# Kernel tuning notes

Measured on AMD Instinct MI355X. Metric: run time of the kernel, lower is better.

Reference implementation:

```python
import jax, jax.numpy as jnp
import numpy as np

B_SZ = 512; S = 3; F = 5; C = 62; E = 5
D_MODEL = C * E * F          # 1550
N_LAYERS = 2
D_STATE = 16
EXPAND = 2
D_CONV = 4
ED = EXPAND * D_MODEL        # 3100
DT_RANK = (D_MODEL + 15) // 16  # 97
VOCAB = 128
EPS = 1e-5


def setup_inputs() -> dict:
    key = jax.random.key(0)
    ks = jax.random.split(key, 10)
    def g(i, shape, scale=0.02):
        return jax.random.normal(ks[i], shape, dtype=jnp.float32) * scale
    A_log = jnp.tile(jnp.log(jnp.arange(1, D_STATE + 1, dtype=jnp.float32))[None, None, :],
                     (N_LAYERS, ED, 1))
    return {
        "x": jax.random.normal(ks[0], (B_SZ, S, F, C, E), dtype=jnp.float32),
        "in_proj_w": g(1, (N_LAYERS, 2 * ED, D_MODEL)),
        "conv_w": g(2, (N_LAYERS, ED, 1, D_CONV), 0.1),
        "conv_b": jnp.zeros((N_LAYERS, ED), jnp.float32),
        "x_proj_w": g(3, (N_LAYERS, DT_RANK + 2 * D_STATE, ED)),
        "dt_proj_w": g(4, (N_LAYERS, ED, DT_RANK), 0.1),
        "dt_proj_b": jnp.full((N_LAYERS, ED), -4.6, jnp.float32),  # softplus ~ 0.01
        "A_log": A_log,
        "D_param": jnp.ones((N_LAYERS, ED), jnp.float32),
        "out_proj_w": g(5, (N_LAYERS, D_MODEL, ED)),
        "norm_w": jnp.ones((N_LAYERS, D_MODEL), jnp.float32),
        "normf_w": jnp.ones((D_MODEL,), jnp.float32),
        "lm_head_w": g(6, (VOCAB, D_MODEL)),
        "bn_w": jnp.ones((F,), jnp.float32),
        "bn_b": jnp.zeros((F,), jnp.float32),
        "emb_w": g(7, (256, VOCAB)),
        "emb_b": jnp.zeros((256,), jnp.float32),
    }


def _rmsnorm(x, w):
    return x * jax.lax.rsqrt(jnp.mean(x * x, axis=-1, keepdims=True) + EPS) * w


def _silu(x):
    return x * jax.nn.sigmoid(x)


def _causal_conv(xt, w, b):
    # xt: (B, ED, L); w: (ED, 1, K) depthwise causal conv (pad K-1 left)
    y = jax.lax.conv_general_dilated(xt, w, (1,), [(D_CONV - 1, 0)],
                                     feature_group_count=ED)
    return y + b[None, :, None]


def _ssm_scan(deltaA, deltaBx, Cm):
    # deltaA, deltaBx: (B, L, ED, N); Cm: (B, L, N)
    def step(h, inp):
        dA, dBx, c = inp
        h = dA * h + dBx                      # (B, ED, N)
        y = jnp.einsum('ben,bn->be', h, c)    # (B, ED)
        return h, y
    h0 = jnp.zeros((deltaA.shape[0], ED, D_STATE), deltaA.dtype)
    xs = (deltaA.transpose(1, 0, 2, 3), deltaBx.transpose(1, 0, 2, 3), Cm.transpose(1, 0, 2))
    _, ys = jax.lax.scan(step, h0, xs)
    return ys.transpose(1, 0, 2)              # (B, L, ED)


def _mixer(h, in_w, cw, cb, xp_w, dt_w, dt_b, A_log, Dp, out_w):
    # h: (B, L, D_MODEL)
    xz = jnp.einsum('bld,ed->ble', h, in_w)   # (B, L, 2*ED)
    x_in, z = jnp.split(xz, 2, axis=-1)
    xc = _silu(_causal_conv(x_in.transpose(0, 2, 1), cw, cb).transpose(0, 2, 1))  # (B,L,ED)
    dbc = jnp.einsum('ble,re->blr', xc, xp_w)  # (B, L, DT_RANK + 2N)
    dt = dbc[..., :DT_RANK]
    Bm = dbc[..., DT_RANK:DT_RANK + D_STATE]
    Cm = dbc[..., DT_RANK + D_STATE:]
    delta = jax.nn.softplus(jnp.einsum('blr,er->ble', dt, dt_w) + dt_b)  # (B,L,ED)
    A = -jnp.exp(A_log)                       # (ED, N)
    deltaA = jnp.exp(delta[..., None] * A)                       # (B,L,ED,N)
    deltaBx = delta[..., None] * Bm[:, :, None, :] * xc[..., None]
    y = _ssm_scan(deltaA, deltaBx, Cm) + Dp * xc
    return jnp.einsum('ble,de->bld', y * _silu(z), out_w)


def reference(x, in_proj_w, conv_w, conv_b, x_proj_w, dt_proj_w, dt_proj_b,
              A_log, D_param, out_proj_w, norm_w, normf_w, lm_head_w,
              bn_w, bn_b, emb_w, emb_b):
    b, s, f, c, e = x.shape
    fx = x.transpose(0, 1, 3, 2, 4).reshape(b, s, c * f * e)  # (B, S, D_MODEL)
    h = fx
    for l in range(N_LAYERS):
        h = h + _mixer(_rmsnorm(h, norm_w[l]), in_proj_w[l], conv_w[l], conv_b[l],
                       x_proj_w[l], dt_proj_w[l], dt_proj_b[l], A_log[l],
                       D_param[l], out_proj_w[l])
    h = _rmsnorm(h, normf_w)
    logits = jnp.einsum('bsd,vd->bsv', h, lm_head_w)          # (B, S, 128)
    m = jnp.broadcast_to(logits[:, None], (b, f, s, VOCAB))    # repeat over f
    # BatchNorm2d(feature_dim) in training mode: stats over (B, S, VOCAB) per channel f
    mean = jnp.mean(m, axis=(0, 2, 3), keepdims=True)
    var = jnp.var(m, axis=(0, 2, 3), keepdims=True)
    mn = (m - mean) * jax.lax.rsqrt(var + EPS)
    mn = mn * bn_w[None, :, None, None] + bn_b[None, :, None, None]
    return jnp.einsum('bfsv,ov->bfso', mn, emb_w) + emb_b      # (B, F, S, 256)
```

## Files before the change

kernel.cpp:

```cpp
#include <hip/hip_runtime.h>
#include <hip/hip_bf16.h>
#include <math.h>

#define B_SZ 512
#define SEQ 3
#define D_MODEL 1550
#define ED 3100
#define NSTATE 16
#define DTR 97
#define DBC_R 129
#define VOCAB 128
#define NBS (B_SZ*SEQ)
#define EPSV 1e-5f

#define KD 1600
#define KE 3136
#define NIP 6272
#define NXP 256
#define NOP 1664
#define NDT 3200
#define KDT 128
#define DBC_LD 256

#define QIP 2508800
#define QXP 200704
#define QDT 102400
#define QOP 1304576
#define AEL 49600
#define QDB 98304
#define QLM 51200
#define QLG 49152
#define TEL 32768
#define PREP_N0 4397762
#define PREP_N1 4264384

static inline int cdiv_h(int a, int b){ return (a + b - 1) / b; }

__device__ __forceinline__ float silu_f(float x){ return x / (1.0f + expf(-x)); }

using bf16x8 = __attribute__((ext_vector_type(8))) short;
using f32x4  = __attribute__((ext_vector_type(4))) float;

__device__ __forceinline__ void gload16(const void* g, void* l){
  __builtin_amdgcn_global_load_lds(
      (const __attribute__((address_space(1))) unsigned int*)g,
      (__attribute__((address_space(3))) unsigned int*)l,
      16, 0, 0);
}

__global__ void k_permute(const float* __restrict__ x, float* __restrict__ h){
  int idx = blockIdx.x * 256 + threadIdx.x;
  if (idx >= NBS * D_MODEL) return;
  int d = idx % D_MODEL;
  int row = idx / D_MODEL;
  int e = d % 5;
  int f = (d / 5) % 5;
  int c = d / 25;
  h[idx] = x[(((size_t)row * 5 + f) * 62 + c) * 5 + e];
}

__device__ __forceinline__ void cast4(const float* __restrict__ src,
                                      __hip_bfloat16* __restrict__ dst,
                                      int q, int N, int K, int Kp){
  int i4 = q * 4;
  int row = i4 / Kp;
  int col = i4 % Kp;
  const float* srow = src + (size_t)row * K;
  #pragma unroll
  for (int j = 0; j < 4; j++){
    int c = col + j;
    float v = (row < N && c < K) ? srow[c] : 0.f;
    dst[i4 + j] = __float2bfloat16(v);
  }
}

__global__ __launch_bounds__(256)
void k_prep(const float* __restrict__ ipw, const float* __restrict__ xpw,
            const float* __restrict__ dtw, const float* __restrict__ opw,
            const float* __restrict__ alog,
            const float* __restrict__ lmw, const float* __restrict__ embw,
            __hip_bfloat16* __restrict__ ipb, __hip_bfloat16* __restrict__ xpb,
            __hip_bfloat16* __restrict__ dtwb, __hip_bfloat16* __restrict__ opb,
            float* __restrict__ A_t, float* __restrict__ dbc,
            __hip_bfloat16* __restrict__ lmb, float* __restrict__ logits,
            float* __restrict__ emb_t, float* __restrict__ sumw,
            float* __restrict__ stats, int l0){
  int idx = blockIdx.x * 256 + threadIdx.x;
  if (idx < QIP){ cast4(ipw, ipb, idx, 2 * ED, D_MODEL, KD); return; } idx -= QIP;
  if (idx < QXP){ cast4(xpw, xpb, idx, DBC_R, ED, KE); return; } idx -= QXP;
  if (idx < QDT){ cast4(dtw, dtwb, idx, ED, DTR, KDT); return; } idx -= QDT;
  if (idx < QOP){ cast4(opw, opb, idx, D_MODEL, ED, KE); return; } idx -= QOP;
  if (idx < AEL){
    int n = idx / ED, ch = idx % ED;
    A_t[idx] = -expf(alog[(size_t)ch * NSTATE + n]);
    return;
  } idx -= AEL;
  if (idx < QDB){
    int i4 = idx * 4;
    dbc[i4] = 0.f; dbc[i4+1] = 0.f; dbc[i4+2] = 0.f; dbc[i4+3] = 0.f;
    return;
  } idx -= QDB;
  if (!l0) return;
  if (idx < QLM){ cast4(lmw, lmb, idx, VOCAB, D_MODEL, KD); return; } idx -= QLM;
  if (idx < QLG){
    int i4 = idx * 4;
    logits[i4] = 0.f; logits[i4+1] = 0.f; logits[i4+2] = 0.f; logits[i4+3] = 0.f;
    return;
  } idx -= QLG;
  if (idx < TEL){
    int v = idx >> 8, o = idx & 255;
    emb_t[idx] = embw[(size_t)o * VOCAB + v];
    return;
  } idx -= TEL;
  if (idx < 256){
    const float* r = embw + (size_t)idx * VOCAB;
    float s = 0.f;
    for (int v = 0; v < VOCAB; v++) s += r[v];
    sumw[idx] = s;
    return;
  } idx -= 256;
  if (idx < 2) stats[idx] = 0.f;
}

__global__ void k_rmsnorm_bf16(const float* __restrict__ in, const float* __restrict__ w,
                               __hip_bfloat16* __restrict__ out, int D, int Kp){
  int row = blockIdx.x;
  const float* xr = in + (size_t)row * D;
  float ss = 0.f;
  for (int i = threadIdx.x; i < D; i += blockDim.x){ float v = xr[i]; ss = fmaf(v, v, ss); }
  __shared__ float red[4];
  __shared__ float sscale;
  int lane = threadIdx.x & 63, wv = threadIdx.x >> 6;
  #pragma unroll
  for (int o = 32; o > 0; o >>= 1) ss += __shfl_down(ss, o, 64);
  if (lane == 0) red[wv] = ss;
  __syncthreads();
  if (threadIdx.x == 0){
    float t = red[0] + red[1] + red[2] + red[3];
    sscale = 1.0f / sqrtf(t / (float)D + EPSV);
  }
  __syncthreads();
  float sc = sscale;
  __hip_bfloat16* orow = out + (size_t)row * Kp;
  for (int i = threadIdx.x; i < Kp; i += blockDim.x){
    float v = (i < D) ? xr[i] * sc * w[i] : 0.f;
    orow[i] = __float2bfloat16(v);
  }
}

__global__ void k_cast_dbc(const float* __restrict__ dbc, __hip_bfloat16* __restrict__ dst){
  int idx = blockIdx.x * 256 + threadIdx.x;
  if (idx >= NBS * KDT) return;
  int row = idx >> 7;
  int c = idx & 127;
  float v = (c < DTR) ? dbc[(size_t)row * DBC_LD + c] : 0.f;
  dst[idx] = __float2bfloat16(v);
}

template<int SPLITS, bool ATOMIC, bool OUT_BF16>
__global__ __launch_bounds__(256)
void k_gemm2(const __hip_bfloat16* __restrict__ A, const __hip_bfloat16* __restrict__ B,
             void* Cv, int Kp, int Nld, int Nreal){
  __shared__ short Al[2][4096];
  __shared__ short Bl[2][4096];
  const int gx = gridDim.x, gy = gridDim.y;
  const int nwg = gx * gy;
  const int wg = blockIdx.y * gx + blockIdx.x;
  const int q = nwg >> 3, r = nwg & 7;
  const int xcd = wg & 7, off = wg >> 3;
  const int nid = (xcd < r ? xcd * (q + 1) : r * (q + 1) + (xcd - r) * q) + off;
  const int bm = (nid % gy) * 128;
  const int bn = (nid / gy) * 128;

  const int t = threadIdx.x;
  const int tt8 = t * 8;

  int kb = 0, ke = Kp;
  if (SPLITS > 1){
    int Kc = ((Kp / SPLITS + 31) / 32) * 32;
    kb = blockIdx.z * Kc;
    ke = min(kb + Kc, Kp);
    if (kb >= ke) return;
  }
  const int nt = (ke - kb) / 32;

  const short* Ab = (const short*)A;
  const short* Bb = (const short*)B;
  const short* ga0 = Ab + (size_t)(bm + (t >> 2)) * Kp + (t & 3) * 8;
  const short* ga1 = Ab + (size_t)(bm + 64 + (t >> 2)) * Kp + (t & 3) * 8;
  const short* gb0 = Bb + (size_t)(bn + (t >> 2)) * Kp + (t & 3) * 8;
  const short* gb1 = Bb + (size_t)(bn + 64 + (t >> 2)) * Kp + (t & 3) * 8;

  const int l = t & 63;
  const int wid = t >> 6;
  const int wr = wid >> 1, wc = wid & 1;
  const int fr = l & 15;
  const int ko = (l >> 4) * 8;

  f32x4 acc[4][4] = {};

#define STAGE(buf, kof) do{ \
    gload16(ga0 + (kof), &Al[buf][tt8]); \
    gload16(ga1 + (kof), &Al[buf][2048 + tt8]); \
    gload16(gb0 + (kof), &Bl[buf][tt8]); \
    gload16(gb1 + (kof), &Bl[buf][2048 + tt8]); }while(0)

  STAGE(0, kb);
  __syncthreads();
  int cur = 0;
  for (int it = 0; it < nt; ++it){
    if (it + 1 < nt) STAGE(cur ^ 1, kb + (it + 1) * 32);
    bf16x8 af[4], bfr[4];
    #pragma unroll
    for (int m = 0; m < 4; m++)
      af[m] = *(const bf16x8*)&Al[cur][(wr * 64 + m * 16 + fr) * 32 + ko];
    #pragma unroll
    for (int n = 0; n < 4; n++)
      bfr[n] = *(const bf16x8*)&Bl[cur][(wc * 64 + n * 16 + fr) * 32 + ko];
    #pragma unroll
    for (int m = 0; m < 4; m++)
      #pragma unroll
      for (int n = 0; n < 4; n++)
        acc[m][n] = __builtin_amdgcn_mfma_f32_16x16x32_bf16(af[m], bfr[n], acc[m][n], 0, 0, 0);
    if (it + 1 < nt){ __syncthreads(); cur ^= 1; }
  }
#undef STAGE

  float* Cf = (float*)Cv;
  __hip_bfloat16* Cb = (__hip_bfloat16*)Cv;
  const int r0 = (l >> 4) * 4;
  #pragma unroll
  for (int m = 0; m < 4; m++){
    #pragma unroll
    for (int n = 0; n < 4; n++){
      int col = bn + wc * 64 + n * 16 + fr;
      if (col < Nreal){
        size_t base = (size_t)(bm + wr * 64 + m * 16 + r0) * Nld + col;
        #pragma unroll
        for (int j = 0; j < 4; j++){
          float v = acc[m][n][j];
          size_t o = base + (size_t)j * Nld;
          if (OUT_BF16)      Cb[o] = __float2bfloat16(v);
          else if (ATOMIC)   atomicAdd(&Cf[o], v);
          else               Cf[o] = v;
        }
      }
    }
  }
}

__global__ void k_conv_silu(const __hip_bfloat16* __restrict__ xz, const float* __restrict__ cw,
                            const float* __restrict__ cb, float* __restrict__ xc_f,
                            __hip_bfloat16* __restrict__ xc_b){
  int idx = blockIdx.x * 256 + threadIdx.x;
  if (idx >= B_SZ * KE) return;
  int ch = idx % KE;
  int b  = idx / KE;
  size_t ob = (size_t)b * SEQ * KE + ch;
  if (ch >= ED){
    __hip_bfloat16 z = __float2bfloat16(0.f);
    xc_b[ob] = z; xc_b[ob + KE] = z; xc_b[ob + 2 * KE] = z;
    return;
  }
  const __hip_bfloat16* base = xz + (size_t)b * SEQ * NIP + ch;
  float x0 = __bfloat162float(base[0]);
  float x1 = __bfloat162float(base[NIP]);
  float x2 = __bfloat162float(base[2 * NIP]);
  const float* w = cw + (size_t)ch * 4;
  float w1 = w[1], w2 = w[2], w3 = w[3];
  float bb = cb[ch];
  float s0 = silu_f(fmaf(w3, x0, bb));
  float s1 = silu_f(fmaf(w2, x0, fmaf(w3, x1, bb)));
  float s2 = silu_f(fmaf(w1, x0, fmaf(w2, x1, fmaf(w3, x2, bb))));
  size_t of = (size_t)b * SEQ * ED + ch;
  xc_f[of]          = s0;
  xc_f[of + ED]     = s1;
  xc_f[of + 2 * ED] = s2;
  xc_b[ob]          = __float2bfloat16(s0);
  xc_b[ob + KE]     = __float2bfloat16(s1);
  xc_b[ob + 2 * KE] = __float2bfloat16(s2);
}

__global__ __launch_bounds__(256)
void k_scan2(const __hip_bfloat16* __restrict__ delta_b, const float* __restrict__ dbc,
             const float* __restrict__ dtb, const float* __restrict__ A_t,
             const float* __restrict__ Dp, const __hip_bfloat16* __restrict__ xz,
             const float* __restrict__ xc_f, __hip_bfloat16* __restrict__ xc_b){
  __shared__ float sB[SEQ][NSTATE], sC[SEQ][NSTATE];
  int b = blockIdx.y;
  if (threadIdx.x < SEQ * 2 * NSTATE){
    int t = threadIdx.x / (2 * NSTATE), r = threadIdx.x % (2 * NSTATE);
    float v = dbc[(size_t)(b * SEQ + t) * DBC_LD + DTR + r];
    if (r < NSTATE) sB[t][r] = v; else sC[t][r - NSTATE] = v;
  }
  __syncthreads();
  int ch = blockIdx.x * 256 + threadIdx.x;
  if (ch >= ED) return;

  float bias = dtb[ch];
  float dlt[SEQ];
  #pragma unroll
  for (int t = 0; t < SEQ; t++){
    float acc = __bfloat162float(delta_b[(size_t)(b * SEQ + t) * NDT + ch]) + bias;
    dlt[t] = (acc > 20.f) ? acc : log1pf(expf(acc));
  }

  size_t of = (size_t)b * SEQ * ED + ch;
  float xcv[SEQ] = { xc_f[of], xc_f[of + ED], xc_f[of + 2 * ED] };
  float y[SEQ] = {0.f, 0.f, 0.f};
  #pragma unroll
  for (int n = 0; n < NSTATE; n++){
    float Av = A_t[(size_t)n * ED + ch];
    float hs = 0.f;
    #pragma unroll
    for (int t = 0; t < SEQ; t++){
      float dA = expf(dlt[t] * Av);
      hs = fmaf(dA, hs, dlt[t] * sB[t][n] * xcv[t]);
      y[t] = fmaf(hs, sC[t][n], y[t]);
    }
  }
  float dp = Dp[ch];
  const __hip_bfloat16* zbase = xz + (size_t)b * SEQ * NIP + ED + ch;
  size_t ob = (size_t)b * SEQ * KE + ch;
  #pragma unroll
  for (int t = 0; t < SEQ; t++){
    float z = __bfloat162float(zbase[(size_t)t * NIP]);
    float yy = fmaf(dp, xcv[t], y[t]);
    xc_b[ob + (size_t)t * KE] = __float2bfloat16(yy * silu_f(z));
  }
}

__global__ __launch_bounds__(256)
void k_stats_part(const float* __restrict__ logits, float* __restrict__ stats){
  float s = 0.f, ss = 0.f;
  for (int i = blockIdx.x * 256 + threadIdx.x; i < NBS * VOCAB; i += gridDim.x * 256){
    float v = logits[i]; s += v; ss = fmaf(v, v, ss);
  }
  #pragma unroll
  for (int o = 32; o > 0; o >>= 1){ s += __shfl_down(s, o, 64); ss += __shfl_down(ss, o, 64); }
  __shared__ float rs[4], rss[4];
  int lane = threadIdx.x & 63, wv = threadIdx.x >> 6;
  if (lane == 0){ rs[wv] = s; rss[wv] = ss; }
  __syncthreads();
  if (threadIdx.x == 0){
    atomicAdd(&stats[0], rs[0] + rs[1] + rs[2] + rs[3]);
    atomicAdd(&stats[1], rss[0] + rss[1] + rss[2] + rss[3]);
  }
}

__global__ __launch_bounds__(256)
void k_projfinal(const float* __restrict__ logits, const float* __restrict__ emb_t,
                 const float* __restrict__ sumw, const float* __restrict__ stats,
                 const float* __restrict__ bnw, const float* __restrict__ bnb,
                 const float* __restrict__ embb, float* __restrict__ out){
  __shared__ float row[VOCAB];
  int r = blockIdx.x;
  int o = threadIdx.x;
  if (o < VOCAB) row[o] = logits[(size_t)r * VOCAB + o];
  __syncthreads();
  float p = 0.f;
  #pragma unroll 8
  for (int v = 0; v < VOCAB; v++) p = fmaf(row[v], emb_t[v * 256 + o], p);
  const float invN = 1.0f / (float)(NBS * VOCAB);
  float mean = stats[0] * invN;
  float var  = stats[1] * invN - mean * mean;
  float rstd = rsqrtf(var + EPSV);
  int b = r / SEQ, s = r % SEQ;
  float sw = sumw[o];
  float base = rstd * (p - mean * sw);
  float eb = embb[o];
  #pragma unroll
  for (int f = 0; f < 5; f++){
    out[(((size_t)(b * 5 + f)) * SEQ + s) * 256 + o] = bnw[f] * base + bnb[f] * sw + eb;
  }
}

extern "C" void kernel_launch(void* const* d_in, const int* in_sizes, int n_in,
                              void* d_out, int out_size, void* d_ws, size_t ws_size,
                              hipStream_t stream) {
  const float* x          = (const float*)d_in[0];
  const float* in_proj_w  = (const float*)d_in[1];
  const float* conv_w     = (const float*)d_in[2];
  const float* conv_b     = (const float*)d_in[3];
  const float* x_proj_w   = (const float*)d_in[4];
  const float* dt_proj_w  = (const float*)d_in[5];
  const float* dt_proj_b  = (const float*)d_in[6];
  const float* A_log      = (const float*)d_in[7];
  const float* D_param    = (const float*)d_in[8];
  const float* out_proj_w = (const float*)d_in[9];
  const float* norm_w     = (const float*)d_in[10];
  const float* normf_w    = (const float*)d_in[11];
  const float* lm_head_w  = (const float*)d_in[12];
  const float* bn_w       = (const float*)d_in[13];
  const float* bn_b       = (const float*)d_in[14];
  const float* emb_w      = (const float*)d_in[15];
  const float* emb_b      = (const float*)d_in[16];

  float* ws = (float*)d_ws;
  float* h      = ws;
  float* xc_f   = h      + (size_t)NBS * D_MODEL;
  float* dbc    = xc_f   + (size_t)NBS * ED;
  float* logits = dbc    + (size_t)NBS * DBC_LD;
  float* sumw   = logits + (size_t)NBS * VOCAB;
  float* stats  = sumw   + 256;
  float* A_t    = stats  + 2;
  float* emb_t  = A_t    + (size_t)NSTATE * ED;
  __hip_bfloat16* xz_b   = (__hip_bfloat16*)(emb_t + (size_t)VOCAB * 256);
  __hip_bfloat16* hn_b   = xz_b   + (size_t)NBS * NIP;
  __hip_bfloat16* xc_b   = hn_b   + (size_t)NBS * KD;
  __hip_bfloat16* dbc_b  = xc_b   + (size_t)NBS * KE;
  __hip_bfloat16* dlt_b  = dbc_b  + (size_t)NBS * KDT;
  __hip_bfloat16* ipb    = dlt_b  + (size_t)NBS * NDT;
  __hip_bfloat16* xpb    = ipb    + (size_t)NIP * KD;
  __hip_bfloat16* dtwb   = xpb    + (size_t)NXP * KE;
  __hip_bfloat16* opb    = dtwb   + (size_t)NDT * KDT;
  __hip_bfloat16* lmb    = opb    + (size_t)NOP * KE;
  size_t need = (size_t)((char*)(lmb + (size_t)VOCAB * KD) - (char*)ws);
  if (ws_size < need) return;

  k_permute<<<cdiv_h(NBS * D_MODEL, 256), 256, 0, stream>>>(x, h);

  for (int l = 0; l < 2; l++){
    const float* ipw = in_proj_w  + (size_t)l * 2 * ED * D_MODEL;
    const float* cw  = conv_w     + (size_t)l * ED * 4;
    const float* cb  = conv_b     + (size_t)l * ED;
    const float* xpw = x_proj_w   + (size_t)l * DBC_R * ED;
    const float* dtw = dt_proj_w  + (size_t)l * ED * DTR;
    const float* dtb = dt_proj_b  + (size_t)l * ED;
    const float* al  = A_log      + (size_t)l * ED * NSTATE;
    const float* dp  = D_param    + (size_t)l * ED;
    const float* opw = out_proj_w + (size_t)l * D_MODEL * ED;
    const float* nw  = norm_w     + (size_t)l * D_MODEL;

    k_prep<<<cdiv_h(l == 0 ? PREP_N0 : PREP_N1, 256), 256, 0, stream>>>(
        ipw, xpw, dtw, opw, al, lm_head_w, emb_w,
        ipb, xpb, dtwb, opb, A_t, dbc, lmb, logits, emb_t, sumw, stats, l == 0 ? 1 : 0);

    k_rmsnorm_bf16<<<NBS, 256, 0, stream>>>(h, nw, hn_b, D_MODEL, KD);

    k_gemm2<1, false, true><<<dim3(NIP / 128, NBS / 128, 1), 256, 0, stream>>>(
        hn_b, ipb, xz_b, KD, NIP, NIP);

    k_conv_silu<<<cdiv_h(B_SZ * KE, 256), 256, 0, stream>>>(xz_b, cw, cb, xc_f, xc_b);

    k_gemm2<8, true, false><<<dim3(NXP / 128, NBS / 128, 8), 256, 0, stream>>>(
        xc_b, xpb, dbc, KE, DBC_LD, DBC_LD);

    k_cast_dbc<<<cdiv_h(NBS * KDT, 256), 256, 0, stream>>>(dbc, dbc_b);
    k_gemm2<1, false, true><<<dim3(NDT / 128, NBS / 128, 1), 256, 0, stream>>>(
        dbc_b, dtwb, dlt_b, KDT, NDT, NDT);

    k_scan2<<<dim3(cdiv_h(ED, 256), B_SZ), 256, 0, stream>>>(
        dlt_b, dbc, dtb, A_t, dp, xz_b, xc_f, xc_b);

    k_gemm2<2, true, false><<<dim3(NOP / 128, NBS / 128, 2), 256, 0, stream>>>(
        xc_b, opb, h, KE, D_MODEL, D_MODEL);
  }

  k_rmsnorm_bf16<<<NBS, 256, 0, stream>>>(h, normf_w, hn_b, D_MODEL, KD);
  k_gemm2<4, true, false><<<dim3(1, NBS / 128, 4), 256, 0, stream>>>(
      hn_b, lmb, logits, KD, VOCAB, VOCAB);

  k_stats_part<<<192, 256, 0, stream>>>(logits, stats);
  k_projfinal<<<NBS, 256, 0, stream>>>(logits, emb_t, sumw, stats,
                                       bn_w, bn_b, emb_b, (float*)d_out);
}
```

Measured before the change: 550.7 us.

## Swizzle GEMM LDS layout, replace atomic split-K with partial buffers, drop fp32 xc

After: 570.3 us. 3.6% more time.

```diff
diff --git a/kernel.cpp b/kernel.cpp
--- a/kernel.cpp
+++ b/kernel.cpp
@@ -27,12 +27,10 @@
 #define QDT 102400
 #define QOP 1304576
 #define AEL 49600
-#define QDB 98304
 #define QLM 51200
-#define QLG 49152
 #define TEL 32768
-#define PREP_N0 4397762
-#define PREP_N1 4264384
+#define PREP_N1 4166080
+#define PREP_N0 4250306
 
 static inline int cdiv_h(int a, int b){ return (a + b - 1) / b; }
 
@@ -81,8 +79,8 @@
             const float* __restrict__ lmw, const float* __restrict__ embw,
             __hip_bfloat16* __restrict__ ipb, __hip_bfloat16* __restrict__ xpb,
             __hip_bfloat16* __restrict__ dtwb, __hip_bfloat16* __restrict__ opb,
-            float* __restrict__ A_t, float* __restrict__ dbc,
-            __hip_bfloat16* __restrict__ lmb, float* __restrict__ logits,
+            float* __restrict__ A_t,
+            __hip_bfloat16* __restrict__ lmb,
             float* __restrict__ emb_t, float* __restrict__ sumw,
             float* __restrict__ stats, int l0){
   int idx = blockIdx.x * 256 + threadIdx.x;
@@ -95,18 +93,8 @@
     A_t[idx] = -expf(alog[(size_t)ch * NSTATE + n]);
     return;
   } idx -= AEL;
-  if (idx < QDB){
-    int i4 = idx * 4;
-    dbc[i4] = 0.f; dbc[i4+1] = 0.f; dbc[i4+2] = 0.f; dbc[i4+3] = 0.f;
-    return;
-  } idx -= QDB;
   if (!l0) return;
   if (idx < QLM){ cast4(lmw, lmb, idx, VOCAB, D_MODEL, KD); return; } idx -= QLM;
-  if (idx < QLG){
-    int i4 = idx * 4;
-    logits[i4] = 0.f; logits[i4+1] = 0.f; logits[i4+2] = 0.f; logits[i4+3] = 0.f;
-    return;
-  } idx -= QLG;
   if (idx < TEL){
     int v = idx >> 8, o = idx & 255;
     emb_t[idx] = embw[(size_t)o * VOCAB + v];
@@ -148,16 +136,7 @@
   }
 }
 
-__global__ void k_cast_dbc(const float* __restrict__ dbc, __hip_bfloat16* __restrict__ dst){
-  int idx = blockIdx.x * 256 + threadIdx.x;
-  if (idx >= NBS * KDT) return;
-  int row = idx >> 7;
-  int c = idx & 127;
-  float v = (c < DTR) ? dbc[(size_t)row * DBC_LD + c] : 0.f;
-  dst[idx] = __float2bfloat16(v);
-}
-
-template<int SPLITS, bool ATOMIC, bool OUT_BF16>
+template<int SPLITS, bool ATOMIC, bool OUT_BF16, bool PARTIAL>
 __global__ __launch_bounds__(256)
 void k_gemm2(const __hip_bfloat16* __restrict__ A, const __hip_bfloat16* __restrict__ B,
              void* Cv, int Kp, int Nld, int Nreal){
@@ -184,18 +163,19 @@
   }
   const int nt = (ke - kb) / 32;
 
+  const int cg = ((t & 3) ^ ((t >> 2) & 3)) * 8;
   const short* Ab = (const short*)A;
   const short* Bb = (const short*)B;
-  const short* ga0 = Ab + (size_t)(bm + (t >> 2)) * Kp + (t & 3) * 8;
-  const short* ga1 = Ab + (size_t)(bm + 64 + (t >> 2)) * Kp + (t & 3) * 8;
-  const short* gb0 = Bb + (size_t)(bn + (t >> 2)) * Kp + (t & 3) * 8;
-  const short* gb1 = Bb + (size_t)(bn + 64 + (t >> 2)) * Kp + (t & 3) * 8;
+  const short* ga0 = Ab + (size_t)(bm + (t >> 2)) * Kp + cg;
+  const short* ga1 = Ab + (size_t)(bm + 64 + (t >> 2)) * Kp + cg;
+  const short* gb0 = Bb + (size_t)(bn + (t >> 2)) * Kp + cg;
+  const short* gb1 = Bb + (size_t)(bn + 64 + (t >> 2)) * Kp + cg;
 
   const int l = t & 63;
   const int wid = t >> 6;
   const int wr = wid >> 1, wc = wid & 1;
   const int fr = l & 15;
-  const int ko = (l >> 4) * 8;
+  const int cc = ((l >> 4) ^ (l & 3)) * 8;
 
   f32x4 acc[4][4] = {};
 
@@ -213,10 +193,10 @@
     bf16x8 af[4], bfr[4];
     #pragma unroll
     for (int m = 0; m < 4; m++)
-      af[m] = *(const bf16x8*)&Al[cur][(wr * 64 + m * 16 + fr) * 32 + ko];
+      af[m] = *(const bf16x8*)&Al[cur][(wr * 64 + m * 16 + fr) * 32 + cc];
     #pragma unroll
     for (int n = 0; n < 4; n++)
-      bfr[n] = *(const bf16x8*)&Bl[cur][(wc * 64 + n * 16 + fr) * 32 + ko];
+      bfr[n] = *(const bf16x8*)&Bl[cur][(wc * 64 + n * 16 + fr) * 32 + cc];
     #pragma unroll
     for (int m = 0; m < 4; m++)
       #pragma unroll
@@ -228,6 +208,8 @@
 
   float* Cf = (float*)Cv;
   __hip_bfloat16* Cb = (__hip_bfloat16*)Cv;
+  const size_t pstride = (size_t)gy * 128 * Nld;
+  if (PARTIAL) Cf += (size_t)blockIdx.z * pstride;
   const int r0 = (l >> 4) * 4;
   #pragma unroll
   for (int m = 0; m < 4; m++){
@@ -250,8 +232,7 @@
 }
 
 __global__ void k_conv_silu(const __hip_bfloat16* __restrict__ xz, const float* __restrict__ cw,
-                            const float* __restrict__ cb, float* __restrict__ xc_f,
-                            __hip_bfloat16* __restrict__ xc_b){
+                            const float* __restrict__ cb, __hip_bfloat16* __restrict__ xc_b){
   int idx = blockIdx.x * 256 + threadIdx.x;
   if (idx >= B_SZ * KE) return;
   int ch = idx % KE;
@@ -272,20 +253,29 @@
   float s0 = silu_f(fmaf(w3, x0, bb));
   float s1 = silu_f(fmaf(w2, x0, fmaf(w3, x1, bb)));
   float s2 = silu_f(fmaf(w1, x0, fmaf(w2, x1, fmaf(w3, x2, bb))));
-  size_t of = (size_t)b * SEQ * ED + ch;
-  xc_f[of]          = s0;
-  xc_f[of + ED]     = s1;
-  xc_f[of + 2 * ED] = s2;
   xc_b[ob]          = __float2bfloat16(s0);
   xc_b[ob + KE]     = __float2bfloat16(s1);
   xc_b[ob + 2 * KE] = __float2bfloat16(s2);
 }
 
 __global__ __launch_bounds__(256)
+void k_xred(const float* __restrict__ part, float* __restrict__ dbc,
+            __hip_bfloat16* __restrict__ dbc_b){
+  int idx = blockIdx.x * 256 + threadIdx.x;
+  if (idx >= NBS * DBC_LD) return;
+  float s = 0.f;
+  #pragma unroll
+  for (int p = 0; p < 8; p++) s += part[(size_t)p * NBS * DBC_LD + idx];
+  dbc[idx] = s;
+  int c = idx & 255, row = idx >> 8;
+  if (c < KDT) dbc_b[(size_t)row * KDT + c] = __float2bfloat16(c < DTR ? s : 0.f);
+}
+
+__global__ __launch_bounds__(256)
 void k_scan2(const __hip_bfloat16* __restrict__ delta_b, const float* __restrict__ dbc,
              const float* __restrict__ dtb, const float* __restrict__ A_t,
              const float* __restrict__ Dp, const __hip_bfloat16* __restrict__ xz,
-             const float* __restrict__ xc_f, __hip_bfloat16* __restrict__ xc_b){
+             __hip_bfloat16* __restrict__ xc_b){
   __shared__ float sB[SEQ][NSTATE], sC[SEQ][NSTATE];
   int b = blockIdx.y;
   if (threadIdx.x < SEQ * 2 * NSTATE){
@@ -305,8 +295,10 @@
     dlt[t] = (acc > 20.f) ? acc : log1pf(expf(acc));
   }
 
-  size_t of = (size_t)b * SEQ * ED + ch;
-  float xcv[SEQ] = { xc_f[of], xc_f[of + ED], xc_f[of + 2 * ED] };
+  size_t ob = (size_t)b * SEQ * KE + ch;
+  float xcv[SEQ] = { __bfloat162float(xc_b[ob]),
+                     __bfloat162float(xc_b[ob + KE]),
+                     __bfloat162float(xc_b[ob + 2 * KE]) };
   float y[SEQ] = {0.f, 0.f, 0.f};
   #pragma unroll
   for (int n = 0; n < NSTATE; n++){
@@ -321,7 +313,6 @@
   }
   float dp = Dp[ch];
   const __hip_bfloat16* zbase = xz + (size_t)b * SEQ * NIP + ED + ch;
-  size_t ob = (size_t)b * SEQ * KE + ch;
   #pragma unroll
   for (int t = 0; t < SEQ; t++){
     float z = __bfloat162float(zbase[(size_t)t * NIP]);
@@ -331,10 +322,15 @@
 }
 
 __global__ __launch_bounds__(256)
-void k_stats_part(const float* __restrict__ logits, float* __restrict__ stats){
+void k_statsred(const float* __restrict__ part, float* __restrict__ logits,
+                float* __restrict__ stats){
   float s = 0.f, ss = 0.f;
   for (int i = blockIdx.x * 256 + threadIdx.x; i < NBS * VOCAB; i += gridDim.x * 256){
-    float v = logits[i]; s += v; ss = fmaf(v, v, ss);
+    float v = 0.f;
+    #pragma unroll
+    for (int p = 0; p < 4; p++) v += part[(size_t)p * NBS * VOCAB + i];
+    logits[i] = v;
+    s += v; ss = fmaf(v, v, ss);
   }
   #pragma unroll
   for (int o = 32; o > 0; o >>= 1){ s += __shfl_down(s, o, 64); ss += __shfl_down(ss, o, 64); }
@@ -398,14 +394,15 @@
 
   float* ws = (float*)d_ws;
   float* h      = ws;
-  float* xc_f   = h      + (size_t)NBS * D_MODEL;
-  float* dbc    = xc_f   + (size_t)NBS * ED;
+  float* dbc    = h      + (size_t)NBS * D_MODEL;
   float* logits = dbc    + (size_t)NBS * DBC_LD;
   float* sumw   = logits + (size_t)NBS * VOCAB;
   float* stats  = sumw   + 256;
   float* A_t    = stats  + 2;
   float* emb_t  = A_t    + (size_t)NSTATE * ED;
-  __hip_bfloat16* xz_b   = (__hip_bfloat16*)(emb_t + (size_t)VOCAB * 256);
+  float* xpart  = emb_t  + (size_t)VOCAB * 256;
+  float* lmpart = xpart  + (size_t)8 * NBS * DBC_LD;
+  __hip_bfloat16* xz_b   = (__hip_bfloat16*)(lmpart + (size_t)4 * NBS * VOCAB);
   __hip_bfloat16* hn_b   = xz_b   + (size_t)NBS * NIP;
   __hip_bfloat16* xc_b   = hn_b   + (size_t)NBS * KD;
   __hip_bfloat16* dbc_b  = xc_b   + (size_t)NBS * KE;
@@ -434,34 +431,34 @@
 
     k_prep<<<cdiv_h(l == 0 ? PREP_N0 : PREP_N1, 256), 256, 0, stream>>>(
         ipw, xpw, dtw, opw, al, lm_head_w, emb_w,
-        ipb, xpb, dtwb, opb, A_t, dbc, lmb, logits, emb_t, sumw, stats, l == 0 ? 1 : 0);
+        ipb, xpb, dtwb, opb, A_t, lmb, emb_t, sumw, stats, l == 0 ? 1 : 0);
 
     k_rmsnorm_bf16<<<NBS, 256, 0, stream>>>(h, nw, hn_b, D_MODEL, KD);
 
-    k_gemm2<1, false, true><<<dim3(NIP / 128, NBS / 128, 1), 256, 0, stream>>>(
+    k_gemm2<1, false, true, false><<<dim3(NIP / 128, NBS / 128, 1), 256, 0, stream>>>(
         hn_b, ipb, xz_b, KD, NIP, NIP);
 
-    k_conv_silu<<<cdiv_h(B_SZ * KE, 256), 256, 0, stream>>>(xz_b, cw, cb, xc_f, xc_b);
-
-    k_gemm2<8, true, false><<<dim3(NXP / 128, NBS / 128, 8), 256, 0, stream>>>(
-        xc_b, xpb, dbc, KE, DBC_LD, DBC_LD);
-
-    k_cast_dbc<<<cdiv_h(NBS * KDT, 256), 256, 0, stream>>>(dbc, dbc_b);
-    k_gemm2<1, false, true><<<dim3(NDT / 128, NBS / 128, 1), 256, 0, stream>>>(
+    k_conv_silu<<<cdiv_h(B_SZ * KE, 256), 256, 0, stream>>>(xz_b, cw, cb, xc_b);
+
+    k_gemm2<8, false, false, true><<<dim3(NXP / 128, NBS / 128, 8), 256, 0, stream>>>(
+        xc_b, xpb, xpart, KE, DBC_LD, DBC_LD);
+    k_xred<<<cdiv_h(NBS * DBC_LD, 256), 256, 0, stream>>>(xpart, dbc, dbc_b);
+
+    k_gemm2<1, false, true, false><<<dim3(NDT / 128, NBS / 128, 1), 256, 0, stream>>>(
         dbc_b, dtwb, dlt_b, KDT, NDT, NDT);
 
     k_scan2<<<dim3(cdiv_h(ED, 256), B_SZ), 256, 0, stream>>>(
-        dlt_b, dbc, dtb, A_t, dp, xz_b, xc_f, xc_b);
-
-    k_gemm2<2, true, false><<<dim3(NOP / 128, NBS / 128, 2), 256, 0, stream>>>(
+        dlt_b, dbc, dtb, A_t, dp, xz_b, xc_b);
+
+    k_gemm2<4, true, false, false><<<dim3(NOP / 128, NBS / 128, 4), 256, 0, stream>>>(
         xc_b, opb, h, KE, D_MODEL, D_MODEL);
   }
 
   k_rmsnorm_bf16<<<NBS, 256, 0, stream>>>(h, normf_w, hn_b, D_MODEL, KD);
-  k_gemm2<4, true, false><<<dim3(1, NBS / 128, 4), 256, 0, stream>>>(
-      hn_b, lmb, logits, KD, VOCAB, VOCAB);
-
-  k_stats_part<<<192, 256, 0, stream>>>(logits, stats);
+  k_gemm2<4, false, false, true><<<dim3(1, NBS / 128, 4), 256, 0, stream>>>(
+      hn_b, lmb, lmpart, KD, VOCAB, VOCAB);
+  k_statsred<<<192, 256, 0, stream>>>(lmpart, logits, stats);
+
   k_projfinal<<<NBS, 256, 0, stream>>>(logits, emb_t, sumw, stats,
                                        bn_w, bn_b, emb_b, (float*)d_out);
 }
```
